# Performance work log

Measured on AMD Instinct MI355X. Metric: run time of the kernel, lower is better.

The kernel has to match this reference:

```python
import jax, jax.numpy as jnp
import numpy as np

N_EMB = 1024
N_HEAD = 16
HEAD_DIM = N_EMB // N_HEAD


def setup_inputs() -> dict:
    key = jax.random.key(0)
    ks = jax.random.split(key, 5)
    scale = 0.02
    x = jax.random.normal(ks[0], (2, 2048, N_EMB), dtype=jnp.float32)
    W_attn = jax.random.normal(ks[1], (N_EMB, 3 * N_EMB), dtype=jnp.float32) * scale
    b_attn = jnp.zeros((3 * N_EMB,), dtype=jnp.float32)
    W_proj = jax.random.normal(ks[2], (N_EMB, N_EMB), dtype=jnp.float32) * scale
    b_proj = jnp.zeros((N_EMB,), dtype=jnp.float32)
    return {"x": x, "W_attn": W_attn, "b_attn": b_attn, "W_proj": W_proj, "b_proj": b_proj}


def reference(x, W_attn, b_attn, W_proj, b_proj):
    B, T, C = x.shape
    qkv = x @ W_attn + b_attn  # [B, T, 3C]
    q, k, v = jnp.split(qkv, 3, axis=-1)
    # [B, H, T, Dh]
    q = q.reshape(B, T, N_HEAD, HEAD_DIM).transpose(0, 2, 1, 3)
    k = k.reshape(B, T, N_HEAD, HEAD_DIM).transpose(0, 2, 1, 3)
    v = v.reshape(B, T, N_HEAD, HEAD_DIM).transpose(0, 2, 1, 3)
    scale = 1.0 / jnp.sqrt(jnp.float32(HEAD_DIM))
    attn = jnp.einsum('bhqd,bhkd->bhqk', q, k) * scale  # [B, H, T, T]
    causal = jnp.tril(jnp.ones((T, T), dtype=bool))
    attn = jnp.where(causal[None, None], attn, -jnp.inf)
    attn = jax.nn.softmax(attn, axis=-1)
    y = jnp.einsum('bhqk,bhkd->bhqd', attn, v)  # [B, H, T, Dh]
    y = y.transpose(0, 2, 1, 3).reshape(B, T, C)
    return y @ W_proj + b_proj
```

## Files before the change

kernel.cpp:

```cpp
#include <hip/hip_runtime.h>
#include <hip/hip_bf16.h>

typedef __bf16 bf16;
typedef __attribute__((ext_vector_type(2))) __bf16 bf16x2;
typedef __attribute__((ext_vector_type(4))) __bf16 bf16x4;
typedef __attribute__((ext_vector_type(8))) __bf16 bf16x8;
typedef __attribute__((ext_vector_type(4))) float f32x4;
typedef __attribute__((ext_vector_type(16))) float f32x16;
typedef unsigned int u32;
typedef __attribute__((ext_vector_type(4))) u32 u32x4;
typedef const __attribute__((address_space(1))) u32* gptr_t;
typedef __attribute__((address_space(3))) u32* lptr_t;

#define N_EMB 1024
#define N_HEAD 16
#define HEAD_DIM 64
#define T_SEQ 2048
#define BATCH 2
#define M_TOT (BATCH * T_SEQ)
#define N_QKV (3 * N_EMB)
#define KDIM 1024
#define CS_LOG2E 0.1803368801111129f

__device__ inline unsigned short f2bu(float f) {
    unsigned u = __builtin_bit_cast(unsigned, f);
    return (unsigned short)((u + 0x7fffu + ((u >> 16) & 1u)) >> 16);
}
__device__ inline bf16 f2b(float f) {
    unsigned short s = f2bu(f);
    return __builtin_bit_cast(bf16, s);
}
__device__ inline u32 pkbf(float lo, float hi) {
    bf16x2 t; t[0] = (bf16)lo; t[1] = (bf16)hi;
    return __builtin_bit_cast(u32, t);
}
__device__ __forceinline__ float xhalf_sum(float x) {
    return x + __shfl_xor(x, 32, 64);
}
__device__ __forceinline__ void lds_fence() {
    asm volatile("s_waitcnt lgkmcnt(0)" ::: "memory");
    __builtin_amdgcn_sched_barrier(0);
}

__global__ __launch_bounds__(256) void k_prep(const float* __restrict__ x,
                                              const float* __restrict__ W_attn,
                                              const float* __restrict__ W_proj,
                                              bf16* __restrict__ xb,
                                              bf16* __restrict__ wat,
                                              bf16* __restrict__ wpt) {
    const int id = blockIdx.x;
    if (id < 4096) {
        int i = id * 256 + threadIdx.x;
        float4 v = reinterpret_cast<const float4*>(x)[i];
        ushort4 u;
        u.x = f2bu(v.x); u.y = f2bu(v.y); u.z = f2bu(v.z); u.w = f2bu(v.w);
        reinterpret_cast<ushort4*>(xb)[i] = u;
        return;
    }
    __shared__ float tile[32][33];
    const float* W; bf16* Wt; int N, bid;
    if (id < 7168) { W = W_attn; Wt = wat; N = N_QKV; bid = id - 4096; }
    else           { W = W_proj; Wt = wpt; N = N_EMB; bid = id - 7168; }
    const int k0 = (bid & 31) * 32;
    const int n0 = (bid >> 5) * 32;
    const int tx = threadIdx.x & 31;
    const int ty = threadIdx.x >> 5;
    for (int j = 0; j < 32; j += 8)
        tile[ty + j][tx] = W[(k0 + ty + j) * N + n0 + tx];
    __syncthreads();
    for (int j = 0; j < 32; j += 8)
        Wt[(n0 + ty + j) * (long)KDIM + k0 + tx] = f2b(tile[tx][ty + j]);
}

__global__ __launch_bounds__(256) void k_vtrans(const bf16* __restrict__ v,
                                                bf16* __restrict__ vt) {
    __shared__ bf16 tile[64 * 76];
    const int bh = blockIdx.y;
    const int t0 = blockIdx.x * 64;
    const bf16* src = v + (size_t)bh * T_SEQ * HEAD_DIM;
    bf16* dst = vt + (size_t)bh * HEAD_DIM * T_SEQ;
    const int tid = threadIdx.x;
    #pragma unroll
    for (int it = 0; it < 2; ++it) {
        const int row = (tid >> 3) + it * 32;
        const int col = (tid & 7) * 8;
        bf16x8 val = *reinterpret_cast<const bf16x8*>(src + (size_t)(t0 + row) * HEAD_DIM + col);
        bf16x4 lo;  lo[0] = val[0]; lo[1] = val[1]; lo[2] = val[2]; lo[3] = val[3];
        bf16x4 hiv; hiv[0] = val[4]; hiv[1] = val[5]; hiv[2] = val[6]; hiv[3] = val[7];
        *reinterpret_cast<bf16x4*>(&tile[row * 76 + col]) = lo;
        *reinterpret_cast<bf16x4*>(&tile[row * 76 + col + 4]) = hiv;
    }
    __syncthreads();
    #pragma unroll
    for (int it = 0; it < 2; ++it) {
        const int d  = (tid >> 3) + it * 32;
        const int tt = (tid & 7) * 8;
        bf16x8 val;
        #pragma unroll
        for (int q = 0; q < 8; ++q) {
            const int pq = tt + q;
            const int sw = ((pq >> 2) ^ (pq >> 3)) & 1;
            const int ps = sw ? (pq ^ 12) : pq;
            val[q] = tile[ps * 76 + d];
        }
        *reinterpret_cast<bf16x8*>(dst + (size_t)d * T_SEQ + t0 + tt) = val;
    }
}

#define GEMM_MAINLOOP(A_, Bt_, m0_, n0_)                                          \
    __shared__ __align__(16) bf16 As[128 * 32];                                   \
    __shared__ __align__(16) bf16 Bs[128 * 32];                                   \
    const int lane = threadIdx.x & 63;                                            \
    const int w    = threadIdx.x >> 6;                                            \
    const int wr   = w >> 1;                                                      \
    const int wc   = w & 1;                                                       \
    const int r    = lane & 15;                                                   \
    const int ko   = (lane >> 4) * 8;                                             \
    const int srow = w * 32 + (lane >> 2);                                        \
    const int sk   = (lane & 3) * 8;                                              \
    const bf16* a_g0 = A_ + (size_t)(m0_ + srow) * KDIM + sk;                     \
    const bf16* a_g1 = a_g0 + 16 * KDIM;                                          \
    const bf16* b_g0 = Bt_ + (size_t)(n0_ + srow) * KDIM + sk;                    \
    const bf16* b_g1 = b_g0 + 16 * KDIM;                                          \
    bf16* a_l0 = As + (w * 2) * 512;                                              \
    bf16* a_l1 = As + (w * 2 + 1) * 512;                                          \
    bf16* b_l0 = Bs + (w * 2) * 512;                                              \
    bf16* b_l1 = Bs + (w * 2 + 1) * 512;                                          \
    f32x4 acc[4][4];                                                              \
    for (int i = 0; i < 4; ++i)                                                   \
        for (int j = 0; j < 4; ++j) acc[i][j] = (f32x4){0.f, 0.f, 0.f, 0.f};      \
    for (int k0 = 0; k0 < KDIM; k0 += 32) {                                       \
        __builtin_amdgcn_global_load_lds((gptr_t)(const void*)(a_g0 + k0),        \
                                         (lptr_t)(void*)a_l0, 16, 0, 0);          \
        __builtin_amdgcn_global_load_lds((gptr_t)(const void*)(a_g1 + k0),        \
                                         (lptr_t)(void*)a_l1, 16, 0, 0);          \
        __builtin_amdgcn_global_load_lds((gptr_t)(const void*)(b_g0 + k0),        \
                                         (lptr_t)(void*)b_l0, 16, 0, 0);          \
        __builtin_amdgcn_global_load_lds((gptr_t)(const void*)(b_g1 + k0),        \
                                         (lptr_t)(void*)b_l1, 16, 0, 0);          \
        __syncthreads();                                                          \
        bf16x8 af[4], bfr[4];                                                     \
        for (int m = 0; m < 4; ++m)                                               \
            af[m] = *reinterpret_cast<const bf16x8*>(As + (wr * 64 + m * 16 + r) * 32 + ko); \
        for (int n = 0; n < 4; ++n)                                               \
            bfr[n] = *reinterpret_cast<const bf16x8*>(Bs + (wc * 64 + n * 16 + r) * 32 + ko); \
        for (int m = 0; m < 4; ++m)                                               \
            for (int n = 0; n < 4; ++n)                                           \
                acc[m][n] = __builtin_amdgcn_mfma_f32_16x16x32_bf16(af[m], bfr[n], acc[m][n], 0, 0, 0); \
        __syncthreads();                                                          \
    }

__global__ __launch_bounds__(256) void k_gemm_qkv(const bf16* __restrict__ A,
                                                  const bf16* __restrict__ Bt,
                                                  const float* __restrict__ bias,
                                                  bf16* __restrict__ qb,
                                                  bf16* __restrict__ kb,
                                                  bf16* __restrict__ vb) {
    const int m0 = blockIdx.x * 128;
    const int n0 = blockIdx.y * 128;
    GEMM_MAINLOOP(A, Bt, m0, n0)
    const int col   = lane & 15;
    const int rbase = (lane >> 4) * 4;
    for (int nn = 0; nn < 4; ++nn) {
        int n = n0 + wc * 64 + nn * 16 + col;
        float bv = bias[n];
        int which = n >> 10;
        int c  = n & 1023;
        int h  = c >> 6;
        int dh = c & 63;
        bf16* dst = (which == 0) ? qb : ((which == 1) ? kb : vb);
        const float sc = (which == 0) ? CS_LOG2E : 1.0f;
        for (int mm = 0; mm < 4; ++mm) {
            for (int i = 0; i < 4; ++i) {
                int m = m0 + wr * 64 + mm * 16 + rbase + i;
                int b_ = m >> 11;
                int t  = m & 2047;
                dst[(((b_ * N_HEAD + h) * T_SEQ) + t) * HEAD_DIM + dh] =
                    f2b((acc[mm][nn][i] + bv) * sc);
            }
        }
    }
}

__global__ __launch_bounds__(256) void k_gemm_proj(const bf16* __restrict__ A,
                                                   const bf16* __restrict__ Bt,
                                                   const float* __restrict__ bias,
                                                   float* __restrict__ out) {
    const int m0 = blockIdx.x * 128;
    const int n0 = blockIdx.y * 128;
    GEMM_MAINLOOP(A, Bt, m0, n0)
    const int col   = lane & 15;
    const int rbase = (lane >> 4) * 4;
    for (int nn = 0; nn < 4; ++nn) {
        int n = n0 + wc * 64 + nn * 16 + col;
        float bv = bias[n];
        for (int mm = 0; mm < 4; ++mm) {
            for (int i = 0; i < 4; ++i) {
                int m = m0 + wr * 64 + mm * 16 + rbase + i;
                out[(size_t)m * N_EMB + n] = acc[mm][nn][i] + bv;
            }
        }
    }
}

__device__ __forceinline__ void pv_group(const float* p,
                                         const bf16x8 (&va)[2][2], f32x16 (&o)[2]) {
    u32x4 f0, f1;
    f0[0] = pkbf(p[0], p[1]);   f0[1] = pkbf(p[2], p[3]);
    f0[2] = pkbf(p[4], p[5]);   f0[3] = pkbf(p[6], p[7]);
    f1[0] = pkbf(p[8], p[9]);   f1[1] = pkbf(p[10], p[11]);
    f1[2] = pkbf(p[12], p[13]); f1[3] = pkbf(p[14], p[15]);
    bf16x8 pb0 = __builtin_bit_cast(bf16x8, f0);
    bf16x8 pb1 = __builtin_bit_cast(bf16x8, f1);
    __builtin_amdgcn_s_setprio(1);
    #pragma unroll
    for (int dt = 0; dt < 2; ++dt) {
        o[dt] = __builtin_amdgcn_mfma_f32_32x32x16_bf16(va[dt][0], pb0, o[dt], 0, 0, 0);
        o[dt] = __builtin_amdgcn_mfma_f32_32x32x16_bf16(va[dt][1], pb1, o[dt], 0, 0, 0);
    }
    __builtin_amdgcn_s_setprio(0);
}

__device__ __forceinline__ void stage_k32(const char* Kg, char* Ks, int kbase, int lane) {
    #pragma unroll
    for (int rr = 0; rr < 4; ++rr) {
        const int fb  = rr * 1024 + lane * 16;
        const int row = fb >> 7;
        const int swz = (row & 7) << 4;
        __builtin_amdgcn_global_load_lds(
            (gptr_t)(const void*)(Kg + (size_t)kbase * 128 + (fb ^ swz)),
            (lptr_t)(void*)(Ks + rr * 1024), 16, 0, 0);
    }
}
__device__ __forceinline__ void stage_v32(const char* Vg, char* Vs, int kbase, int lane) {
    #pragma unroll
    for (int rr = 0; rr < 4; ++rr) {
        const int fb  = rr * 1024 + lane * 16;
        const int d   = fb >> 6;
        const int off = fb & 63;
        const int swz = (d & 3) << 4;
        __builtin_amdgcn_global_load_lds(
            (gptr_t)(const void*)(Vg + (size_t)d * (T_SEQ * 2) + (size_t)kbase * 2 + (off ^ swz)),
            (lptr_t)(void*)(Vs + rr * 1024), 16, 0, 0);
    }
}

__device__ __forceinline__ void load_kf(const char* Ks, int qr, int hi, bf16x8 (&kf)[4]) {
    const int swzk = (qr & 7) << 4;
    #pragma unroll
    for (int f = 0; f < 4; ++f)
        kf[f] = *reinterpret_cast<const bf16x8*>(
            Ks + ((qr * 128 + f * 32 + hi * 16) ^ swzk));
}
__device__ __forceinline__ void load_va(const char* Vs, int qr, int hi, bf16x8 (&va)[2][2]) {
    #pragma unroll
    for (int dt = 0; dt < 2; ++dt)
        #pragma unroll
        for (int ks = 0; ks < 2; ++ks) {
            const int d = dt * 32 + qr;
            va[dt][ks] = *reinterpret_cast<const bf16x8*>(
                Vs + ((d * 64 + ks * 32 + hi * 16) ^ ((d & 3) << 4)));
        }
}

__device__ __forceinline__ f32x16 qkt_tile(const bf16x8 (&kf)[4], const bf16x8 (&qf)[4]) {
    f32x16 st;
    #pragma unroll
    for (int r = 0; r < 16; ++r) st[r] = 0.f;
    __builtin_amdgcn_s_setprio(1);
    #pragma unroll
    for (int f = 0; f < 4; ++f)
        st = __builtin_amdgcn_mfma_f32_32x32x16_bf16(kf[f], qf[f], st, 0, 0, 0);
    __builtin_amdgcn_s_setprio(0);
    return st;
}

__device__ __forceinline__ void softmax_pv(f32x16 st, const bf16x8 (&va)[2][2],
                                           int qr, int hi, bool diag,
                                           float& l_r, f32x16 (&o)[2]) {
    if (diag) {
        const int kp4 = 4 * hi;
        #pragma unroll
        for (int r = 0; r < 16; ++r) {
            const int kpos = (r & 3) + 8 * (r >> 2) + kp4;
            if (kpos > qr) st[r] = -3.0e38f;
        }
    }
    float p[16];
    #pragma unroll
    for (int r = 0; r < 16; ++r) p[r] = exp2f(st[r]);
    float s = 0.f;
    #pragma unroll
    for (int r = 0; r < 8; ++r) s += p[r] + p[r + 8];
    l_r += s;
    pv_group(p, va, o);
}

__global__ __launch_bounds__(256) void k_attn(const bf16* __restrict__ qb,
                                              const bf16* __restrict__ kb,
                                              const bf16* __restrict__ vtb,
                                              bf16* __restrict__ yb) {
    const int lane = threadIdx.x & 63;
    const int wv   = threadIdx.x >> 6;
    const int bh   = blockIdx.x;
    const int qblk = 63 - blockIdx.y;
    const int q0   = qblk * 32;
    const int b    = bh >> 4;
    const int h    = bh & 15;

    const char* Qg = (const char*)(qb  + (size_t)bh * T_SEQ * HEAD_DIM);
    const char* Kg = (const char*)(kb  + (size_t)bh * T_SEQ * HEAD_DIM);
    const char* Vg = (const char*)(vtb + (size_t)bh * HEAD_DIM * T_SEQ);

    const int qr = lane & 31;
    const int hi = lane >> 5;

    __shared__ __align__(16) char sbuf[4][8192];
    char* Ks = sbuf[wv];
    char* Vs = sbuf[wv] + 4096;

    stage_k32(Qg, Ks, qblk * 32, lane);
    asm volatile("s_waitcnt vmcnt(0)" ::: "memory");
    bf16x8 qf[4];
    load_kf(Ks, qr, hi, qf);
    lds_fence();

    f32x16 o[2];
    #pragma unroll
    for (int r = 0; r < 16; ++r) { o[0][r] = 0.f; o[1][r] = 0.f; }
    float l_r = 0.f;

    const int n    = qblk + 1;
    const int base = n >> 2;
    const int rem  = n & 3;
    const int lo   = wv * base + (wv < rem ? wv : rem);
    const int cnt  = base + (wv < rem ? 1 : 0);
    const int end  = lo + cnt;

    if (cnt > 0) {
        stage_k32(Kg, Ks, lo * 32, lane);
        stage_v32(Vg, Vs, lo * 32, lane);
        for (int t = lo; t < end; ++t) {
            asm volatile("s_waitcnt vmcnt(4)" ::: "memory");
            bf16x8 kf[4];
            load_kf(Ks, qr, hi, kf);
            f32x16 st = qkt_tile(kf, qf);
            asm volatile("s_waitcnt vmcnt(0)" ::: "memory");
            bf16x8 va[2][2];
            load_va(Vs, qr, hi, va);
            lds_fence();
            if (t + 1 < end) {
                stage_k32(Kg, Ks, (t + 1) * 32, lane);
                stage_v32(Vg, Vs, (t + 1) * 32, lane);
            }
            softmax_pv(st, va, qr, hi, t == qblk, l_r, o);
        }
    }

    if (wv > 0) {
        bf16* so = (bf16*)sbuf[wv];
        #pragma unroll
        for (int i = 0; i < 16; ++i) {
            so[i * 64 + lane]        = f2b(o[0][i]);
            so[(16 + i) * 64 + lane] = f2b(o[1][i]);
        }
        *reinterpret_cast<float*>(sbuf[wv] + 4096 + lane * 4) = l_r;
    }
    __syncthreads();
    if (wv > 0) return;
    #pragma unroll
    for (int s = 1; s < 4; ++s) {
        const bf16* so = (const bf16*)sbuf[s];
        l_r += *reinterpret_cast<const float*>(sbuf[s] + 4096 + lane * 4);
        #pragma unroll
        for (int i = 0; i < 16; ++i) {
            o[0][i] += (float)so[i * 64 + lane];
            o[1][i] += (float)so[(16 + i) * 64 + lane];
        }
    }
    l_r = xhalf_sum(l_r);

    const float inv = 1.f / fmaxf(l_r, 1e-30f);
    const int tq = q0 + qr;
    bf16* yrow = yb + ((size_t)(b * T_SEQ + tq)) * N_EMB + h * HEAD_DIM;
    #pragma unroll
    for (int dt = 0; dt < 2; ++dt) {
        #pragma unroll
        for (int rr = 0; rr < 4; ++rr) {
            const int d0 = dt * 32 + 8 * rr + 4 * hi;
            ushort4 u;
            u.x = f2bu(o[dt][4 * rr + 0] * inv);
            u.y = f2bu(o[dt][4 * rr + 1] * inv);
            u.z = f2bu(o[dt][4 * rr + 2] * inv);
            u.w = f2bu(o[dt][4 * rr + 3] * inv);
            *reinterpret_cast<ushort4*>(yrow + d0) = u;
        }
    }
}

extern "C" void kernel_launch(void* const* d_in, const int* in_sizes, int n_in,
                              void* d_out, int out_size, void* d_ws, size_t ws_size,
                              hipStream_t stream) {
    const float* x      = (const float*)d_in[0];
    const float* W_attn = (const float*)d_in[1];
    const float* b_attn = (const float*)d_in[2];
    const float* W_proj = (const float*)d_in[3];
    const float* b_proj = (const float*)d_in[4];
    float* out = (float*)d_out;

    const size_t sz_x   = (size_t)M_TOT * N_EMB;
    const size_t sz_wat = (size_t)N_QKV * N_EMB;
    const size_t sz_wpt = (size_t)N_EMB * N_EMB;
    const size_t sz_hd  = (size_t)BATCH * N_HEAD * T_SEQ * HEAD_DIM;
    const size_t need = (sz_x + sz_wat + sz_wpt + 3 * sz_hd + sz_x) * sizeof(bf16);
    if (ws_size < need) return;

    bf16* xb  = (bf16*)d_ws;
    bf16* wat = xb + sz_x;
    bf16* wpt = wat + sz_wat;
    bf16* qb  = wpt + sz_wpt;
    bf16* kbf = qb + sz_hd;
    bf16* vbf = kbf + sz_hd;
    bf16* yb  = vbf + sz_hd;
    bf16* vtb = xb;

    k_prep<<<dim3(8192), 256, 0, stream>>>(x, W_attn, W_proj, xb, wat, wpt);
    k_gemm_qkv<<<dim3(M_TOT / 128, N_QKV / 128), 256, 0, stream>>>(xb, wat, b_attn, qb, kbf, vbf);
    k_vtrans<<<dim3(T_SEQ / 64, BATCH * N_HEAD), 256, 0, stream>>>(vbf, vtb);
    k_attn<<<dim3(BATCH * N_HEAD, 64), 256, 0, stream>>>(qb, kbf, vtb, yb);
    k_gemm_proj<<<dim3(M_TOT / 128, N_EMB / 128), 256, 0, stream>>>(yb, wpt, b_proj, out);
}
```

Before: 114.5 us.

## Double-buffer K/V LDS staging in attention kernel to prefetch two tiles ahead

Each wave now has two K/V LDS buffers and prefetches tile t+2 while computing tile t. The goal is to hide global-load latency better than the previous single buffer, which forced a full wait on V before the PV step each iteration. In exchange, per-block LDS doubles to 64KB, which may reduce occupancy, and the waitcnt logic assumes eight outstanding loads per tile.

New measurement: 120.1 us. +4.9%, slower.

```diff
diff --git a/kernel.cpp b/kernel.cpp
--- a/kernel.cpp
+++ b/kernel.cpp
@@ -315,14 +315,16 @@
     const int qr = lane & 31;
     const int hi = lane >> 5;
 
-    __shared__ __align__(16) char sbuf[4][8192];
-    char* Ks = sbuf[wv];
-    char* Vs = sbuf[wv] + 4096;
-
-    stage_k32(Qg, Ks, qblk * 32, lane);
+    __shared__ __align__(16) char sbuf[4][16384];
+    char* Ks0 = sbuf[wv];
+    char* Vs0 = sbuf[wv] + 4096;
+    char* Ks1 = sbuf[wv] + 8192;
+    char* Vs1 = sbuf[wv] + 12288;
+
+    stage_k32(Qg, Ks0, qblk * 32, lane);
     asm volatile("s_waitcnt vmcnt(0)" ::: "memory");
     bf16x8 qf[4];
-    load_kf(Ks, qr, hi, qf);
+    load_kf(Ks0, qr, hi, qf);
     lds_fence();
 
     f32x16 o[2];
@@ -338,20 +340,28 @@
     const int end  = lo + cnt;
 
     if (cnt > 0) {
-        stage_k32(Kg, Ks, lo * 32, lane);
-        stage_v32(Vg, Vs, lo * 32, lane);
+        stage_k32(Kg, Ks0, lo * 32, lane);
+        stage_v32(Vg, Vs0, lo * 32, lane);
+        if (lo + 1 < end) {
+            stage_k32(Kg, Ks1, (lo + 1) * 32, lane);
+            stage_v32(Vg, Vs1, (lo + 1) * 32, lane);
+        }
         for (int t = lo; t < end; ++t) {
-            asm volatile("s_waitcnt vmcnt(4)" ::: "memory");
+            char* Kc = ((t - lo) & 1) ? Ks1 : Ks0;
+            char* Vc = ((t - lo) & 1) ? Vs1 : Vs0;
+            if (t + 1 < end)
+                asm volatile("s_waitcnt vmcnt(8)" ::: "memory");
+            else
+                asm volatile("s_waitcnt vmcnt(0)" ::: "memory");
             bf16x8 kf[4];
-            load_kf(Ks, qr, hi, kf);
+            load_kf(Kc, qr, hi, kf);
             f32x16 st = qkt_tile(kf, qf);
-            asm volatile("s_waitcnt vmcnt(0)" ::: "memory");
             bf16x8 va[2][2];
-            load_va(Vs, qr, hi, va);
+            load_va(Vc, qr, hi, va);
             lds_fence();
-            if (t + 1 < end) {
-                stage_k32(Kg, Ks, (t + 1) * 32, lane);
-                stage_v32(Vg, Vs, (t + 1) * 32, lane);
+            if (t + 2 < end) {
+                stage_k32(Kg, Kc, (t + 2) * 32, lane);
+                stage_v32(Vg, Vc, (t + 2) * 32, lane);
             }
             softmax_pv(st, va, qr, hi, t == qblk, l_r, o);
         }
```
